# Kernel tuning notes

Hardware: AMD Instinct MI355X
Metric: run time of the kernel (lower is better)

The kernel has to match this reference:

```python
import jax, jax.numpy as jnp
import numpy as np

LN_EPS = 1e-5

def setup_inputs() -> dict:
    key = jax.random.key(0)
    ks = jax.random.split(key, 12)
    B, S, M, C, D = 16, 1024, 4096, 768, 256
    inp = {
        'seed_xyz_norm': jax.random.normal(ks[0], (B, S, 3), jnp.float32),
        'p_last': jax.random.normal(ks[1], (B, M, 3), jnp.float32),
        'f_last': jax.random.normal(ks[2], (B, C, M), jnp.float32),
        'seed_features': jax.random.normal(ks[3], (B, D, S), jnp.float32),
        # LayerNorm params over C
        'ln_gamma': jnp.ones((C,), jnp.float32),
        'ln_beta': jnp.zeros((C,), jnp.float32),
        # conv1d projector C -> 256 (kernel size 1) + ReLU
        'proj_w': jax.random.normal(ks[4], (D, C), jnp.float32) * (1.0 / np.sqrt(C)),
        'proj_b': jnp.zeros((D,), jnp.float32),
        # fusion MLP: concat512 -> 512 -> 256 (1x1 convs)
        'mlp_w1': jax.random.normal(ks[5], (2 * D, 2 * D), jnp.float32) * (1.0 / np.sqrt(2 * D)),
        'mlp_b1': jnp.zeros((2 * D,), jnp.float32),
        'mlp_w2': jax.random.normal(ks[6], (D, 2 * D), jnp.float32) * (1.0 / np.sqrt(2 * D)),
        'mlp_b2': jnp.zeros((D,), jnp.float32),
    }
    return inp


def reference(seed_xyz_norm, p_last, f_last, seed_features,
              ln_gamma, ln_beta, proj_w, proj_b,
              mlp_w1, mlp_b1, mlp_w2, mlp_b2):
    # --- nearest_neighbor_gather_features ---
    # squared distance [B,S,M]; argmin over M, gather features [B,C,S]
    d2 = jnp.sum(seed_xyz_norm * seed_xyz_norm, -1, keepdims=True) \
         - 2.0 * jnp.einsum('bsd,bmd->bsm', seed_xyz_norm, p_last) \
         + jnp.sum(p_last * p_last, -1)[:, None, :]
    idx = jnp.argmin(d2, axis=-1)                                   # [B,S]
    lift3d_raw = jnp.take_along_axis(f_last, idx[:, None, :], axis=2)  # [B,C,S]

    # --- LayerNorm over channel dim C ---
    mu = jnp.mean(lift3d_raw, axis=1, keepdims=True)
    var = jnp.mean((lift3d_raw - mu) ** 2, axis=1, keepdims=True)
    x_ln = (lift3d_raw - mu) * jax.lax.rsqrt(var + LN_EPS)
    x_ln = x_ln * ln_gamma[None, :, None] + ln_beta[None, :, None]

    # --- conv1d projector (1x1) + ReLU ---
    proj = jax.nn.relu(jnp.einsum('oc,bcs->bos', proj_w, x_ln) + proj_b[None, :, None])

    # --- concat fusion MLP ---
    fused = jnp.concatenate([seed_features, proj], axis=1)          # [B,512,S]
    h = jax.nn.relu(jnp.einsum('oc,bcs->bos', mlp_w1, fused) + mlp_b1[None, :, None])
    mixed = jnp.einsum('oc,bcs->bos', mlp_w2, h) + mlp_b2[None, :, None]  # [B,256,S]
    return mixed
```

## Files before the change

### kernel.cpp

```cpp
#include <hip/hip_runtime.h>

namespace {

constexpr int B = 16, S = 1024, M = 4096, C = 768, D = 256;

typedef __attribute__((ext_vector_type(8))) short bf16x8;
typedef __attribute__((ext_vector_type(4))) float f32x4;

__device__ inline ushort f2bf(float f) {
  uint u = __float_as_uint(f);
  uint r = (u + 0x7FFFu + ((u >> 16) & 1u)) >> 16;
  return (ushort)r;
}

__global__ __launch_bounds__(256)
void nn_kernel(const float* __restrict__ xyz, const float* __restrict__ p,
               int* __restrict__ idx_out) {
  const int b = blockIdx.y;
  const int t = threadIdx.x;
  const int seed = blockIdx.x * 16 + (t >> 4);
  const int l16 = t & 15;

  const float sx = xyz[((size_t)b * S + seed) * 3 + 0];
  const float sy = xyz[((size_t)b * S + seed) * 3 + 1];
  const float sz = xyz[((size_t)b * S + seed) * 3 + 2];
  const float ss = __fadd_rn(__fadd_rn(__fmul_rn(sx, sx), __fmul_rn(sy, sy)),
                             __fmul_rn(sz, sz));

  __shared__ float px[256], py[256], pz[256], pp[256];

  float best = 3.4028235e38f;
  int besti = 0;
  const float* pb = p + (size_t)b * M * 3;

  for (int m0 = 0; m0 < M; m0 += 256) {
    __syncthreads();
    {
      const float a0 = pb[(size_t)(m0 + t) * 3 + 0];
      const float a1 = pb[(size_t)(m0 + t) * 3 + 1];
      const float a2 = pb[(size_t)(m0 + t) * 3 + 2];
      px[t] = a0; py[t] = a1; pz[t] = a2;
      pp[t] = __fadd_rn(__fadd_rn(__fmul_rn(a0, a0), __fmul_rn(a1, a1)),
                        __fmul_rn(a2, a2));
    }
    __syncthreads();
    #pragma unroll 4
    for (int j = l16; j < 256; j += 16) {
      float dot = __fmul_rn(sx, px[j]);
      dot = __fadd_rn(dot, __fmul_rn(sy, py[j]));
      dot = __fadd_rn(dot, __fmul_rn(sz, pz[j]));
      const float d2 = __fadd_rn(__fsub_rn(ss, __fmul_rn(2.0f, dot)), pp[j]);
      const int mi = m0 + j;
      if (d2 < best || (d2 == best && mi < besti)) { best = d2; besti = mi; }
    }
  }
  #pragma unroll
  for (int off = 8; off >= 1; off >>= 1) {
    const float ob = __shfl_xor(best, off, 16);
    const int   oi = __shfl_xor(besti, off, 16);
    if (ob < best || (ob == best && oi < besti)) { best = ob; besti = oi; }
  }
  if (l16 == 0) idx_out[b * S + seed] = besti;
}

__global__ __launch_bounds__(512)
void sort_kernel(const int* __restrict__ idx, int* __restrict__ sIdx,
                 int* __restrict__ sS) {
  const int b = blockIdx.x;
  const int t = threadIdx.x;
  __shared__ int key[1024];
  __shared__ int val[1024];
  key[t] = idx[b * S + t];         val[t] = t;
  key[t + 512] = idx[b * S + t + 512]; val[t + 512] = t + 512;
  __syncthreads();
  for (int k = 2; k <= 1024; k <<= 1) {
    for (int j = k >> 1; j > 0; j >>= 1) {
      #pragma unroll 2
      for (int i = t; i < 1024; i += 512) {
        const int p = i ^ j;
        if (p > i) {
          const bool up = ((i & k) == 0);
          const int ki = key[i], kp = key[p];
          if ((ki > kp) == up) {
            key[i] = kp; key[p] = ki;
            const int tv = val[i]; val[i] = val[p]; val[p] = tv;
          }
        }
      }
      __syncthreads();
    }
  }
  sIdx[b * S + t] = key[t];       sS[b * S + t] = val[t];
  sIdx[b * S + t + 512] = key[t + 512]; sS[b * S + t + 512] = val[t + 512];
}

__global__ __launch_bounds__(256)
void gather_ln_kernel(const float* __restrict__ f, const int* __restrict__ sIdx,
                      const int* __restrict__ sS,
                      const float* __restrict__ gamma, const float* __restrict__ beta,
                      ushort* __restrict__ xln) {
  const int b = blockIdx.y;
  const int rl = blockIdx.x;
  const int r = ((rl & 7) << 7) + (rl >> 3);
  const int t = threadIdx.x;
  const int s = sS[b * S + r];
  const int m = sIdx[b * S + r];

  const float* fb = f + (size_t)b * C * M + m;
  const float v0 = fb[(size_t)(t      ) * M];
  const float v1 = fb[(size_t)(t + 256) * M];
  const float v2 = fb[(size_t)(t + 512) * M];

  __shared__ float red[4];
  __shared__ float stats[2];
  const int wave = t >> 6;

  float ps = v0 + v1 + v2;
  #pragma unroll
  for (int off = 32; off >= 1; off >>= 1) ps += __shfl_xor(ps, off);
  if ((t & 63) == 0) red[wave] = ps;
  __syncthreads();
  if (t == 0) stats[0] = (red[0] + red[1] + red[2] + red[3]) * (1.0f / 768.0f);
  __syncthreads();
  const float mu = stats[0];

  const float d0 = v0 - mu, d1 = v1 - mu, d2 = v2 - mu;
  float pv = d0 * d0 + d1 * d1 + d2 * d2;
  #pragma unroll
  for (int off = 32; off >= 1; off >>= 1) pv += __shfl_xor(pv, off);
  if ((t & 63) == 0) red[wave] = pv;
  __syncthreads();
  if (t == 0) {
    const float var = (red[0] + red[1] + red[2] + red[3]) * (1.0f / 768.0f);
    stats[1] = 1.0f / sqrtf(var + 1e-5f);
  }
  __syncthreads();
  const float rs = stats[1];

  ushort* ob = xln + ((size_t)b * S + s) * C;
  ob[t      ] = f2bf((d0 * rs) * gamma[t      ] + beta[t      ]);
  ob[t + 256] = f2bf((d1 * rs) * gamma[t + 256] + beta[t + 256]);
  ob[t + 512] = f2bf((d2 * rs) * gamma[t + 512] + beta[t + 512]);
}

__global__ __launch_bounds__(256)
void transpose_sf_kernel(const float* __restrict__ sf, ushort* __restrict__ fused) {
  const int b = blockIdx.z;
  const int d0 = blockIdx.y * 64;
  const int s0 = blockIdx.x * 64;
  const int t = threadIdx.x;
  __shared__ float tile[64][68];

  const float* inb = sf + ((size_t)b * D + d0) * S + s0;
  #pragma unroll
  for (int q = 0; q < 4; ++q) {
    const int rr = (t >> 4) + q * 16;
    const int c4 = (t & 15) * 4;
    const float4 v = *(const float4*)&inb[(size_t)rr * S + c4];
    *(float4*)&tile[rr][c4] = v;
  }
  __syncthreads();
  #pragma unroll
  for (int q = 0; q < 4; ++q) {
    const int srow = (t >> 4) + q * 16;
    const int dc = (t & 15) * 4;
    ushort4 o;
    o.x = f2bf(tile[dc + 0][srow]);
    o.y = f2bf(tile[dc + 1][srow]);
    o.z = f2bf(tile[dc + 2][srow]);
    o.w = f2bf(tile[dc + 3][srow]);
    *(ushort4*)&fused[((size_t)b * S + s0 + srow) * 512 + d0 + dc] = o;
  }
}

__global__ __launch_bounds__(256)
void convert_w_kernel(const float* __restrict__ w0, int n0, ushort* __restrict__ o0,
                      const float* __restrict__ w1, int n1, ushort* __restrict__ o1,
                      const float* __restrict__ w2, int n2, ushort* __restrict__ o2) {
  const int which = blockIdx.y;
  const float* src = which == 0 ? w0 : which == 1 ? w1 : w2;
  ushort* dst = which == 0 ? o0 : which == 1 ? o1 : o2;
  const int n = which == 0 ? n0 : which == 1 ? n1 : n2;
  const int i = (blockIdx.x * 256 + threadIdx.x) * 4;
  if (i < n) {
    const float4 v = *(const float4*)&src[i];
    ushort4 o;
    o.x = f2bf(v.x); o.y = f2bf(v.y); o.z = f2bf(v.z); o.w = f2bf(v.w);
    *(ushort4*)&dst[i] = o;
  }
}

__global__ __launch_bounds__(256)
void gemm_bf16_kernel(const ushort* __restrict__ W, int K, int O,
                      const ushort* __restrict__ X,
                      const float* __restrict__ bias,
                      void* __restrict__ out, int outMode, int ldOut, int colOff,
                      int relu) {
  const int b  = blockIdx.z;
  const int s0 = blockIdx.x * 128;
  const int o0 = blockIdx.y * 128;
  const int t  = threadIdx.x;
  const int wave = t >> 6;
  const int lane = t & 63;
  const int l16 = lane & 15;
  const int quad = lane >> 4;

  __shared__ ushort Wt[128 * 40];
  __shared__ ushort Xt[128 * 40];
  __shared__ float biasS[128];

  if (t < 128) biasS[t] = bias[o0 + t];

  f32x4 acc[8][2];
  const f32x4 z = {0.f, 0.f, 0.f, 0.f};
  #pragma unroll
  for (int of = 0; of < 8; ++of) { acc[of][0] = z; acc[of][1] = z; }

  const ushort* Xb = X + (size_t)b * S * K;
  const int kg = t & 3;
  const int row = t >> 2;

  for (int c0 = 0; c0 < K; c0 += 32) {
    __syncthreads();
    #pragma unroll
    for (int q = 0; q < 2; ++q) {
      const int rr = row + 64 * q;
      const uint4 wv = *(const uint4*)&W[(size_t)(o0 + rr) * K + c0 + kg * 8];
      *(uint4*)&Wt[rr * 40 + kg * 8] = wv;
      const uint4 xv = *(const uint4*)&Xb[(size_t)(s0 + rr) * K + c0 + kg * 8];
      *(uint4*)&Xt[rr * 40 + kg * 8] = xv;
    }
    __syncthreads();

    bf16x8 bfr[2];
    #pragma unroll
    for (int sf = 0; sf < 2; ++sf)
      bfr[sf] = *(const bf16x8*)&Xt[(wave * 32 + sf * 16 + l16) * 40 + quad * 8];
    #pragma unroll
    for (int of = 0; of < 8; ++of) {
      const bf16x8 afr = *(const bf16x8*)&Wt[(of * 16 + l16) * 40 + quad * 8];
      acc[of][0] = __builtin_amdgcn_mfma_f32_16x16x32_bf16(afr, bfr[0], acc[of][0], 0, 0, 0);
      acc[of][1] = __builtin_amdgcn_mfma_f32_16x16x32_bf16(afr, bfr[1], acc[of][1], 0, 0, 0);
    }
  }

  if (outMode == 0) {
    ushort* ob = (ushort*)out;
    #pragma unroll
    for (int of = 0; of < 8; ++of) {
      #pragma unroll
      for (int sf = 0; sf < 2; ++sf) {
        const int s = s0 + wave * 32 + sf * 16 + l16;
        const int ol = of * 16 + quad * 4;
        float v0 = acc[of][sf].x + biasS[ol + 0];
        float v1 = acc[of][sf].y + biasS[ol + 1];
        float v2 = acc[of][sf].z + biasS[ol + 2];
        float v3 = acc[of][sf].w + biasS[ol + 3];
        if (relu) {
          v0 = fmaxf(v0, 0.f); v1 = fmaxf(v1, 0.f);
          v2 = fmaxf(v2, 0.f); v3 = fmaxf(v3, 0.f);
        }
        ushort4 st;
        st.x = f2bf(v0); st.y = f2bf(v1); st.z = f2bf(v2); st.w = f2bf(v3);
        *(ushort4*)&ob[((size_t)b * S + s) * ldOut + colOff + o0 + ol] = st;
      }
    }
  } else {
    float* o32 = (float*)out;
    #pragma unroll
    for (int of = 0; of < 8; ++of) {
      #pragma unroll
      for (int sf = 0; sf < 2; ++sf) {
        const int s = s0 + wave * 32 + sf * 16 + l16;
        const int ol = of * 16 + quad * 4;
        const float vr[4] = {acc[of][sf].x, acc[of][sf].y, acc[of][sf].z, acc[of][sf].w};
        #pragma unroll
        for (int r = 0; r < 4; ++r) {
          const int o = o0 + ol + r;
          o32[((size_t)b * O + o) * S + s] = vr[r] + biasS[ol + r];
        }
      }
    }
  }
}

}

extern "C" void kernel_launch(void* const* d_in, const int* in_sizes, int n_in,
                              void* d_out, int out_size, void* d_ws, size_t ws_size,
                              hipStream_t stream) {
  const float* seed_xyz  = (const float*)d_in[0];
  const float* p_last    = (const float*)d_in[1];
  const float* f_last    = (const float*)d_in[2];
  const float* seed_feat = (const float*)d_in[3];
  const float* ln_gamma  = (const float*)d_in[4];
  const float* ln_beta   = (const float*)d_in[5];
  const float* proj_w    = (const float*)d_in[6];
  const float* proj_b    = (const float*)d_in[7];
  const float* mlp_w1    = (const float*)d_in[8];
  const float* mlp_b1    = (const float*)d_in[9];
  const float* mlp_w2    = (const float*)d_in[10];
  const float* mlp_b2    = (const float*)d_in[11];
  float* out = (float*)d_out;

  char* ws = (char*)d_ws;
  int*    idx   = (int*)(ws);
  int*    sIdx  = (int*)(ws + (64 << 10));
  int*    sS    = (int*)(ws + (128 << 10));
  ushort* wp_bf = (ushort*)(ws + (256 << 10));
  ushort* w1_bf = (ushort*)(ws + (640 << 10));
  ushort* w2_bf = (ushort*)(ws + (1152 << 10));
  ushort* xln   = (ushort*)(ws + (2ull << 20));
  ushort* fused = (ushort*)(ws + (26ull << 20));
  ushort* hbuf  = (ushort*)(ws + (42ull << 20));

  nn_kernel<<<dim3(S / 16, B), 256, 0, stream>>>(seed_xyz, p_last, idx);
  sort_kernel<<<dim3(B), 512, 0, stream>>>(idx, sIdx, sS);

  gather_ln_kernel<<<dim3(S, B), 256, 0, stream>>>(f_last, sIdx, sS,
                                                   ln_gamma, ln_beta, xln);

  transpose_sf_kernel<<<dim3(S / 64, D / 64, B), 256, 0, stream>>>(seed_feat, fused);
  convert_w_kernel<<<dim3(256, 3), 256, 0, stream>>>(
      proj_w, D * C, wp_bf, mlp_w1, 512 * 512, w1_bf, mlp_w2, 256 * 512, w2_bf);

  gemm_bf16_kernel<<<dim3(S / 128, 256 / 128, B), 256, 0, stream>>>(
      wp_bf, C, 256, xln, proj_b, fused, 0, 512, 256, 1);

  gemm_bf16_kernel<<<dim3(S / 128, 512 / 128, B), 256, 0, stream>>>(
      w1_bf, 512, 512, fused, mlp_b1, hbuf, 0, 512, 0, 1);

  gemm_bf16_kernel<<<dim3(S / 128, 256 / 128, B), 256, 0, stream>>>(
      w2_bf, 512, 256, hbuf, mlp_b2, out, 1, 0, 0, 0);
}
```

Before: 434.9 us.

## Coalesce nearest-neighbor gather via tiled transpose and retile GEMM with direct LDS loads

Replaces the per-seed strided gather of f_last with a tiled pass that reads contiguous M-tiles, transposes them in shared memory, and scatters rows for seeds whose nearest index falls in the tile, followed by a separate LayerNorm kernel. The GEMM is retiled to 64x128 over the flattened batch with global_load_lds and an XOR-swizzled LDS layout, plus a float4 LDS layout in the NN search. This trades scattered sector-wasting reads for a full coalesced read of f_last plus an extra fp32 intermediate round trip.

```diff
diff --git a/kernel.cpp b/kernel.cpp
--- a/kernel.cpp
+++ b/kernel.cpp
@@ -3,6 +3,7 @@
 namespace {
 
 constexpr int B = 16, S = 1024, M = 4096, C = 768, D = 256;
+constexpr int N = B * S;
 
 typedef __attribute__((ext_vector_type(8))) short bf16x8;
 typedef __attribute__((ext_vector_type(4))) float f32x4;
@@ -11,6 +12,12 @@
   uint u = __float_as_uint(f);
   uint r = (u + 0x7FFFu + ((u >> 16) & 1u)) >> 16;
   return (ushort)r;
+}
+
+__device__ __forceinline__ void g2lds16(const ushort* g, ushort* l) {
+  __builtin_amdgcn_global_load_lds(
+      (const __attribute__((address_space(1))) uint*)g,
+      (__attribute__((address_space(3))) uint*)l, 16, 0, 0);
 }
 
 __global__ __launch_bounds__(256)
@@ -27,7 +34,7 @@
   const float ss = __fadd_rn(__fadd_rn(__fmul_rn(sx, sx), __fmul_rn(sy, sy)),
                              __fmul_rn(sz, sz));
 
-  __shared__ float px[256], py[256], pz[256], pp[256];
+  __shared__ float4 pt[256];
 
   float best = 3.4028235e38f;
   int besti = 0;
@@ -39,17 +46,18 @@
       const float a0 = pb[(size_t)(m0 + t) * 3 + 0];
       const float a1 = pb[(size_t)(m0 + t) * 3 + 1];
       const float a2 = pb[(size_t)(m0 + t) * 3 + 2];
-      px[t] = a0; py[t] = a1; pz[t] = a2;
-      pp[t] = __fadd_rn(__fadd_rn(__fmul_rn(a0, a0), __fmul_rn(a1, a1)),
-                        __fmul_rn(a2, a2));
+      const float pp = __fadd_rn(__fadd_rn(__fmul_rn(a0, a0), __fmul_rn(a1, a1)),
+                                 __fmul_rn(a2, a2));
+      pt[t] = make_float4(a0, a1, a2, pp);
     }
     __syncthreads();
     #pragma unroll 4
     for (int j = l16; j < 256; j += 16) {
-      float dot = __fmul_rn(sx, px[j]);
-      dot = __fadd_rn(dot, __fmul_rn(sy, py[j]));
-      dot = __fadd_rn(dot, __fmul_rn(sz, pz[j]));
-      const float d2 = __fadd_rn(__fsub_rn(ss, __fmul_rn(2.0f, dot)), pp[j]);
+      const float4 q = pt[j];
+      float dot = __fmul_rn(sx, q.x);
+      dot = __fadd_rn(dot, __fmul_rn(sy, q.y));
+      dot = __fadd_rn(dot, __fmul_rn(sz, q.z));
+      const float d2 = __fadd_rn(__fsub_rn(ss, __fmul_rn(2.0f, dot)), q.w);
       const int mi = m0 + j;
       if (d2 < best || (d2 == best && mi < besti)) { best = d2; besti = mi; }
     }
@@ -70,7 +78,7 @@
   const int t = threadIdx.x;
   __shared__ int key[1024];
   __shared__ int val[1024];
-  key[t] = idx[b * S + t];         val[t] = t;
+  key[t] = idx[b * S + t];             val[t] = t;
   key[t + 512] = idx[b * S + t + 512]; val[t + 512] = t + 512;
   __syncthreads();
   for (int k = 2; k <= 1024; k <<= 1) {
@@ -90,26 +98,66 @@
       __syncthreads();
     }
   }
-  sIdx[b * S + t] = key[t];       sS[b * S + t] = val[t];
+  sIdx[b * S + t] = key[t];             sS[b * S + t] = val[t];
   sIdx[b * S + t + 512] = key[t + 512]; sS[b * S + t + 512] = val[t + 512];
 }
 
 __global__ __launch_bounds__(256)
-void gather_ln_kernel(const float* __restrict__ f, const int* __restrict__ sIdx,
-                      const int* __restrict__ sS,
-                      const float* __restrict__ gamma, const float* __restrict__ beta,
-                      ushort* __restrict__ xln) {
+void gatherT_kernel(const float* __restrict__ f, const int* __restrict__ sIdx,
+                    const int* __restrict__ sS, float* __restrict__ tmp) {
   const int b = blockIdx.y;
-  const int rl = blockIdx.x;
-  const int r = ((rl & 7) << 7) + (rl >> 3);
-  const int t = threadIdx.x;
-  const int s = sS[b * S + r];
-  const int m = sIdx[b * S + r];
-
-  const float* fb = f + (size_t)b * C * M + m;
-  const float v0 = fb[(size_t)(t      ) * M];
-  const float v1 = fb[(size_t)(t + 256) * M];
-  const float v2 = fb[(size_t)(t + 512) * M];
+  const int m0 = blockIdx.x * 64;
+  const int t = threadIdx.x;
+  __shared__ float tile[64][65];
+  __shared__ int bound[2];
+
+  if (t < 2) {
+    const int target = m0 + (t ? 64 : 0);
+    int lo = 0, hi = S;
+    while (lo < hi) {
+      const int mid = (lo + hi) >> 1;
+      if (sIdx[b * S + mid] < target) lo = mid + 1; else hi = mid;
+    }
+    bound[t] = lo;
+  }
+  __syncthreads();
+  const int lo = bound[0];
+  const int cnt = bound[1] - bound[0];
+  if (cnt == 0) return;
+
+  const float* fb = f + (size_t)b * C * M + m0;
+  const int wv = t >> 6;
+  const int ml = t & 63;
+
+  for (int cc = 0; cc < 12; ++cc) {
+    __syncthreads();
+    const int c0 = cc * 64;
+    #pragma unroll
+    for (int q = 0; q < 16; ++q) {
+      const int cl = q * 4 + wv;
+      tile[cl][ml] = fb[(size_t)(c0 + cl) * M + ml];
+    }
+    __syncthreads();
+    for (int i0 = 0; i0 < cnt; i0 += 4) {
+      const int i = i0 + wv;
+      if (i < cnt) {
+        const int r = lo + i;
+        const int mloc = sIdx[b * S + r] - m0;
+        const int s = sS[b * S + r];
+        tmp[((size_t)b * S + s) * C + c0 + ml] = tile[ml][mloc];
+      }
+    }
+  }
+}
+
+__global__ __launch_bounds__(256)
+void ln_kernel(const float* __restrict__ tmp,
+               const float* __restrict__ gamma, const float* __restrict__ beta,
+               ushort* __restrict__ xln) {
+  const int n = blockIdx.y * 1024 + blockIdx.x;
+  const int t = threadIdx.x;
+  const float* row = tmp + (size_t)n * C;
+  const float v0 = row[t], v1 = row[t + 256], v2 = row[t + 512];
 
   __shared__ float red[4];
   __shared__ float stats[2];
@@ -137,7 +185,7 @@
   __syncthreads();
   const float rs = stats[1];
 
-  ushort* ob = xln + ((size_t)b * S + s) * C;
+  ushort* ob = xln + (size_t)n * C;
   ob[t      ] = f2bf((d0 * rs) * gamma[t      ] + beta[t      ]);
   ob[t + 256] = f2bf((d1 * rs) * gamma[t + 256] + beta[t + 256]);
   ob[t + 512] = f2bf((d2 * rs) * gamma[t + 512] + beta[t + 512]);
@@ -190,55 +238,60 @@
   }
 }
 
-__global__ __launch_bounds__(256)
+__global__ __launch_bounds__(256, 2)
 void gemm_bf16_kernel(const ushort* __restrict__ W, int K, int O,
                       const ushort* __restrict__ X,
                       const float* __restrict__ bias,
                       void* __restrict__ out, int outMode, int ldOut, int colOff,
                       int relu) {
-  const int b  = blockIdx.z;
-  const int s0 = blockIdx.x * 128;
+  const int n0 = blockIdx.x * 64;
   const int o0 = blockIdx.y * 128;
-  const int t  = threadIdx.x;
-  const int wave = t >> 6;
+  const int t = threadIdx.x;
+  const int w = t >> 6;
   const int lane = t & 63;
   const int l16 = lane & 15;
   const int quad = lane >> 4;
-
-  __shared__ ushort Wt[128 * 40];
-  __shared__ ushort Xt[128 * 40];
+  const int wo = w >> 1;
+  const int wsd = w & 1;
+
+  __shared__ ushort Wt[128 * 32];
+  __shared__ ushort Xt[64 * 32];
   __shared__ float biasS[128];
-
   if (t < 128) biasS[t] = bias[o0 + t];
 
-  f32x4 acc[8][2];
+  f32x4 acc[4][2];
   const f32x4 z = {0.f, 0.f, 0.f, 0.f};
   #pragma unroll
-  for (int of = 0; of < 8; ++of) { acc[of][0] = z; acc[of][1] = z; }
-
-  const ushort* Xb = X + (size_t)b * S * K;
-  const int kg = t & 3;
-  const int row = t >> 2;
+  for (int of = 0; of < 4; ++of) { acc[of][0] = z; acc[of][1] = z; }
+
+  const int srow = lane >> 2;
+  const int chk = lane & 3;
 
   for (int c0 = 0; c0 < K; c0 += 32) {
     __syncthreads();
     #pragma unroll
     for (int q = 0; q < 2; ++q) {
-      const int rr = row + 64 * q;
-      const uint4 wv = *(const uint4*)&W[(size_t)(o0 + rr) * K + c0 + kg * 8];
-      *(uint4*)&Wt[rr * 40 + kg * 8] = wv;
-      const uint4 xv = *(const uint4*)&Xb[(size_t)(s0 + rr) * K + c0 + kg * 8];
-      *(uint4*)&Xt[rr * 40 + kg * 8] = xv;
+      const int r = w * 32 + q * 16 + srow;
+      const int cc = chk ^ (r & 3);
+      g2lds16(&W[(size_t)(o0 + r) * K + c0 + cc * 8], &Wt[(w * 32 + q * 16) * 32]);
+    }
+    {
+      const int r = w * 16 + srow;
+      const int cc = chk ^ (r & 3);
+      g2lds16(&X[(size_t)(n0 + r) * K + c0 + cc * 8], &Xt[(w * 16) * 32]);
     }
     __syncthreads();
 
     bf16x8 bfr[2];
     #pragma unroll
-    for (int sf = 0; sf < 2; ++sf)
-      bfr[sf] = *(const bf16x8*)&Xt[(wave * 32 + sf * 16 + l16) * 40 + quad * 8];
-    #pragma unroll
-    for (int of = 0; of < 8; ++of) {
-      const bf16x8 afr = *(const bf16x8*)&Wt[(of * 16 + l16) * 40 + quad * 8];
+    for (int sf = 0; sf < 2; ++sf) {
+      const int sr = wsd * 32 + sf * 16 + l16;
+      bfr[sf] = *(const bf16x8*)&Xt[sr * 32 + ((quad ^ (sr & 3)) * 8)];
+    }
+    #pragma unroll
+    for (int of = 0; of < 4; ++of) {
+      const int orr = wo * 64 + of * 16 + l16;
+      const bf16x8 afr = *(const bf16x8*)&Wt[orr * 32 + ((quad ^ (orr & 3)) * 8)];
       acc[of][0] = __builtin_amdgcn_mfma_f32_16x16x32_bf16(afr, bfr[0], acc[of][0], 0, 0, 0);
       acc[of][1] = __builtin_amdgcn_mfma_f32_16x16x32_bf16(afr, bfr[1], acc[of][1], 0, 0, 0);
     }
@@ -247,11 +300,11 @@
   if (outMode == 0) {
     ushort* ob = (ushort*)out;
     #pragma unroll
-    for (int of = 0; of < 8; ++of) {
+    for (int of = 0; of < 4; ++of) {
       #pragma unroll
       for (int sf = 0; sf < 2; ++sf) {
-        const int s = s0 + wave * 32 + sf * 16 + l16;
-        const int ol = of * 16 + quad * 4;
+        const int n = n0 + wsd * 32 + sf * 16 + l16;
+        const int ol = wo * 64 + of * 16 + quad * 4;
         float v0 = acc[of][sf].x + biasS[ol + 0];
         float v1 = acc[of][sf].y + biasS[ol + 1];
         float v2 = acc[of][sf].z + biasS[ol + 2];
@@ -262,22 +315,23 @@
         }
         ushort4 st;
         st.x = f2bf(v0); st.y = f2bf(v1); st.z = f2bf(v2); st.w = f2bf(v3);
-        *(ushort4*)&ob[((size_t)b * S + s) * ldOut + colOff + o0 + ol] = st;
+        *(ushort4*)&ob[(size_t)n * ldOut + colOff + o0 + ol] = st;
       }
     }
   } else {
     float* o32 = (float*)out;
     #pragma unroll
-    for (int of = 0; of < 8; ++of) {
+    for (int of = 0; of < 4; ++of) {
       #pragma unroll
       for (int sf = 0; sf < 2; ++sf) {
-        const int s = s0 + wave * 32 + sf * 16 + l16;
-        const int ol = of * 16 + quad * 4;
+        const int n = n0 + wsd * 32 + sf * 16 + l16;
+        const int ol = wo * 64 + of * 16 + quad * 4;
+        const int bb = n >> 10, s = n & 1023;
         const float vr[4] = {acc[of][sf].x, acc[of][sf].y, acc[of][sf].z, acc[of][sf].w};
         #pragma unroll
         for (int r = 0; r < 4; ++r) {
           const int o = o0 + ol + r;
-          o32[((size_t)b * O + o) * S + s] = vr[r] + biasS[ol + r];
+          o32[((size_t)bb * O + o) * S + s] = vr[r] + biasS[ol + r];
         }
       }
     }
@@ -310,26 +364,27 @@
   ushort* wp_bf = (ushort*)(ws + (256 << 10));
   ushort* w1_bf = (ushort*)(ws + (640 << 10));
   ushort* w2_bf = (ushort*)(ws + (1152 << 10));
-  ushort* xln   = (ushort*)(ws + (2ull << 20));
-  ushort* fused = (ushort*)(ws + (26ull << 20));
-  ushort* hbuf  = (ushort*)(ws + (42ull << 20));
+  float*  tmp   = (float*)(ws + (2ull << 20));
+  ushort* xln   = (ushort*)(ws + (50ull << 20));
+  ushort* fused = (ushort*)(ws + (74ull << 20));
+  ushort* hbuf  = (ushort*)(ws + (90ull << 20));
 
   nn_kernel<<<dim3(S / 16, B), 256, 0, stream>>>(seed_xyz, p_last, idx);
   sort_kernel<<<dim3(B), 512, 0, stream>>>(idx, sIdx, sS);
 
-  gather_ln_kernel<<<dim3(S, B), 256, 0, stream>>>(f_last, sIdx, sS,
-                                                   ln_gamma, ln_beta, xln);
+  gatherT_kernel<<<dim3(M / 64, B), 256, 0, stream>>>(f_last, sIdx, sS, tmp);
+  ln_kernel<<<dim3(1024, B), 256, 0, stream>>>(tmp, ln_gamma, ln_beta, xln);
 
   transpose_sf_kernel<<<dim3(S / 64, D / 64, B), 256, 0, stream>>>(seed_feat, fused);
   convert_w_kernel<<<dim3(256, 3), 256, 0, stream>>>(
       proj_w, D * C, wp_bf, mlp_w1, 512 * 512, w1_bf, mlp_w2, 256 * 512, w2_bf);
 
-  gemm_bf16_kernel<<<dim3(S / 128, 256 / 128, B), 256, 0, stream>>>(
+  gemm_bf16_kernel<<<dim3(N / 64, 256 / 128), 256, 0, stream>>>(
       wp_bf, C, 256, xln, proj_b, fused, 0, 512, 256, 1);
 
-  gemm_bf16_kernel<<<dim3(S / 128, 512 / 128, B), 256, 0, stream>>>(
+  gemm_bf16_kernel<<<dim3(N / 64, 512 / 128), 256, 0, stream>>>(
       w1_bf, 512, 512, fused, mlp_b1, hbuf, 0, 512, 0, 1);
 
-  gemm_bf16_kernel<<<dim3(S / 128, 256 / 128, B), 256, 0, stream>>>(
+  gemm_bf16_kernel<<<dim3(N / 64, 256 / 128), 256, 0, stream>>>(
       w2_bf, 512, 256, hbuf, mlp_b2, out, 1, 0, 0, 0);
 }
```

After: 457.5 us. +5.2%, slower.
